# Performance work log

Measured on AMD Instinct MI355X. Metric: run time of the kernel, lower is better.

The kernel has to match this reference:

```python
import jax, jax.numpy as jnp
import numpy as np

N_GRAPHS = 64
NEG_SLOPE = 0.01  # default LeakyReLU slope
BN_EPS = 1e-5


def setup_inputs() -> dict:
    key = jax.random.key(0)
    ks = jax.random.split(key, 16)
    N, E, F_IN, H, H2, OUT, L = 50000, 800000, 64, 128, 64, 8, 3
    return {
        "x": jax.random.normal(ks[0], (N, F_IN), jnp.float32),
        "edge_index": jax.random.randint(ks[1], (2, E), 0, N, jnp.int32),
        "batch": jnp.sort(jax.random.randint(ks[2], (N,), 0, N_GRAPHS, jnp.int32)),
        "W_emb": jax.random.normal(ks[3], (F_IN, H), jnp.float32) * 0.05,
        "b_emb": jnp.zeros((H,), jnp.float32),
        "convW": jax.random.normal(ks[4], (L, H, H), jnp.float32) * 0.05,
        "convB": jnp.zeros((L, H), jnp.float32),
        "bn_gamma": jax.random.uniform(ks[5], (L, H), jnp.float32) + 0.5,
        "bn_beta": jax.random.normal(ks[6], (L, H), jnp.float32) * 0.1,
        "bn_mean": jax.random.normal(ks[7], (L, H), jnp.float32) * 0.1,
        "bn_var": jax.random.uniform(ks[8], (L, H), jnp.float32) + 0.5,
        "W1": jax.random.normal(ks[9], (H, H2), jnp.float32) * 0.05,
        "b1": jnp.zeros((H2,), jnp.float32),
        "W2": jax.random.normal(ks[10], (H2, OUT), jnp.float32) * 0.05,
        "b2": jnp.zeros((OUT,), jnp.float32),
    }


def reference(x, edge_index, batch, W_emb, b_emb, convW, convB,
              bn_gamma, bn_beta, bn_mean, bn_var, W1, b1, W2, b2):
    N = x.shape[0]
    # GCN normalization with self-loops (computed once; identical per layer)
    loop = jnp.arange(N, dtype=edge_index.dtype)
    s = jnp.concatenate([edge_index[0], loop])  # [E+N]
    d = jnp.concatenate([edge_index[1], loop])
    deg = jax.ops.segment_sum(jnp.ones(d.shape, x.dtype), d, num_segments=N)
    dinv = jax.lax.rsqrt(deg)  # deg >= 1 thanks to self-loops
    norm = dinv[s] * dinv[d]  # [E+N]

    h = x @ W_emb + b_emb  # node embedding, [N, H]
    L = convW.shape[0]
    for i in range(L):
        m = h @ convW[i]  # linear transform, [N, H]
        # gather-weight-scatter: sum_{(s->d)} norm * m[s]
        agg = jax.ops.segment_sum(m[s] * norm[:, None], d, num_segments=N) + convB[i]
        # BatchNorm (eval mode, running stats)
        hbn = (agg - bn_mean[i]) * jax.lax.rsqrt(bn_var[i] + BN_EPS) * bn_gamma[i] + bn_beta[i]
        h = jnp.where(hbn > 0, hbn, NEG_SLOPE * hbn)  # LeakyReLU
        # dropout is identity in eval mode

    g = jax.ops.segment_sum(h, batch, num_segments=N_GRAPHS)  # global_add_pool, [G, H]
    z = g @ W1 + b1
    z = jnp.where(z > 0, z, NEG_SLOPE * z)
    return z @ W2 + b2  # [G, OUT]
```

## Files before the change

kernel.cpp:

```cpp
#include <hip/hip_runtime.h>

#define NEG 0.01f
#define HF 128
#define BK 64
#define CAP 5120

typedef __attribute__((ext_vector_type(8))) short bf8;
typedef __attribute__((ext_vector_type(4))) float f4;

__device__ __forceinline__ unsigned short f2bf(float v) {
    unsigned u = __float_as_uint(v);
    u = (u + 0x7fff + ((u >> 16) & 1)) >> 16;
    return (unsigned short)u;
}

__global__ __launch_bounds__(256) void k_mega1(
        const int* __restrict__ src, const int* __restrict__ dst, int E,
        int* __restrict__ bin_cnt, int2* __restrict__ binbuf,
        const float* __restrict__ x, const float* __restrict__ W_emb,
        const float* __restrict__ b_emb, short* __restrict__ hbuf, int N,
        const float* __restrict__ convW, short* __restrict__ wt_c, int L,
        int PB, int EB) {
    __shared__ short wt[128 * 88];
    __shared__ int hist[256];
    __shared__ int base[256];
    const int bid = blockIdx.x;
    const int tid = threadIdx.x;

    if (bid < PB) {
        const int per = (E + PB - 1) / PB;
        const int e0 = bid * per;
        const int e1 = (e0 + per < E) ? e0 + per : E;
        hist[tid] = 0;
        __syncthreads();
        for (int e = e0 + tid; e < e1; e += 256)
            atomicAdd(&hist[dst[e] >> 8], 1);
        __syncthreads();
        const int h = hist[tid];
        base[tid] = h > 0 ? atomicAdd(&bin_cnt[tid], h) : 0;
        hist[tid] = 0;
        __syncthreads();
        for (int e = e0 + tid; e < e1; e += 256) {
            const int d = dst[e];
            const int b = d >> 8;
            const int slot = base[b] + atomicAdd(&hist[b], 1);
            if (slot < CAP) binbuf[(size_t)b * CAP + slot] = make_int2(src[e], d);
        }
        return;
    }
    if (bid < PB + EB) {
        for (int i = tid; i < 128 * 64; i += 256) {
            const int n = i >> 6, k = i & 63;
            wt[n * 88 + k] = (short)f2bf(W_emb[(size_t)k * HF + n]);
        }
        __syncthreads();
        const int wid = tid >> 6, lane = tid & 63;
        const int lr = lane & 15, lk = lane >> 4;
        const int m0 = (bid - PB) * 64 + wid * 16;
        if (m0 >= N) return;
        const int arow_i = m0 + lr < N ? m0 + lr : N - 1;
        bf8 a[2];
        const float* arow = x + (size_t)arow_i * 64 + lk * 8;
#pragma unroll
        for (int kk = 0; kk < 2; ++kk) {
            const float4 p = *reinterpret_cast<const float4*>(arow + kk * 32);
            const float4 q = *reinterpret_cast<const float4*>(arow + kk * 32 + 4);
            bf8 t;
            t[0] = (short)f2bf(p.x); t[1] = (short)f2bf(p.y);
            t[2] = (short)f2bf(p.z); t[3] = (short)f2bf(p.w);
            t[4] = (short)f2bf(q.x); t[5] = (short)f2bf(q.y);
            t[6] = (short)f2bf(q.z); t[7] = (short)f2bf(q.w);
            a[kk] = t;
        }
#pragma unroll
        for (int n = 0; n < 8; ++n) {
            f4 acc = {0.f, 0.f, 0.f, 0.f};
            const short* brow = wt + (n * 16 + lr) * 88 + lk * 8;
#pragma unroll
            for (int kk = 0; kk < 2; ++kk) {
                const bf8 b = *reinterpret_cast<const bf8*>(brow + kk * 32);
                acc = __builtin_amdgcn_mfma_f32_16x16x32_bf16(a[kk], b, acc, 0, 0, 0);
            }
            const int col = n * 16 + lr;
            const float bs = b_emb[col];
#pragma unroll
            for (int r = 0; r < 4; ++r)
                hbuf[(size_t)(m0 + lk * 4 + r) * HF + col] = (short)f2bf(acc[r] + bs);
        }
        return;
    }
    const int i = (bid - PB - EB) * 256 + tid;
    const int per = HF * HF;
    if (i < L * per) {
        const int l = i / per, r = i % per;
        const int n = r / HF, k = r % HF;
        wt_c[i] = (short)f2bf(convW[(size_t)l * per + (size_t)k * HF + n]);
    }
}

__global__ __launch_bounds__(256) void k_binfill(
        const int* __restrict__ bin_cnt, const int2* __restrict__ binbuf,
        int* __restrict__ bkt, int* __restrict__ cnt,
        float* __restrict__ gbuf, int NBIN) {
    const int bid = blockIdx.x;
    const int tid = threadIdx.x;
    if (bid >= NBIN) {
        for (int i = tid; i < 64 * HF; i += 256) gbuf[i] = 0.0f;
        return;
    }
    __shared__ int lcnt[256];
    lcnt[tid] = 0;
    __syncthreads();
    int count = bin_cnt[bid];
    if (count > CAP) count = CAP;
    for (int e = tid; e < count; e += 256) {
        const int2 ed = binbuf[(size_t)bid * CAP + e];
        const int p = atomicAdd(&lcnt[ed.y & 255], 1);
        if (p < BK) bkt[(size_t)ed.y * BK + p] = ed.x;
    }
    __syncthreads();
    cnt[(bid << 8) + tid] = lcnt[tid];
}

__global__ __launch_bounds__(256) void k_gemm_conv(
        const short* __restrict__ A,
        const short* __restrict__ Bt,
        const int* __restrict__ cnt,
        short* __restrict__ C,
        int N) {
    const int tid = threadIdx.x;
    const int wid = tid >> 6, lane = tid & 63;
    const int lr = lane & 15, lk = lane >> 4;
    const int m0 = blockIdx.x * 128 + wid * 32;
    if (m0 >= N) return;
    bf8 aA[4], aB[4];
    const short* arowA = A + (size_t)(m0 + lr) * HF + lk * 8;
    const short* arowB = arowA + 16 * HF;
#pragma unroll
    for (int kk = 0; kk < 4; ++kk) {
        aA[kk] = *reinterpret_cast<const bf8*>(arowA + kk * 32);
        aB[kk] = *reinterpret_cast<const bf8*>(arowB + kk * 32);
    }
    float dvA[4], dvB[4];
#pragma unroll
    for (int r = 0; r < 4; ++r) {
        int rowA = m0 + lk * 4 + r;       if (rowA >= N) rowA = N - 1;
        int rowB = m0 + 16 + lk * 4 + r;  if (rowB >= N) rowB = N - 1;
        dvA[r] = rsqrtf((float)cnt[rowA] + 1.0f);
        dvB[r] = rsqrtf((float)cnt[rowB] + 1.0f);
    }
#pragma unroll
    for (int n = 0; n < 8; ++n) {
        f4 accA = {0.f, 0.f, 0.f, 0.f};
        f4 accB = {0.f, 0.f, 0.f, 0.f};
        const short* brow = Bt + (size_t)(n * 16 + lr) * HF + lk * 8;
#pragma unroll
        for (int kk = 0; kk < 4; ++kk) {
            const bf8 b = *reinterpret_cast<const bf8*>(brow + kk * 32);
            accA = __builtin_amdgcn_mfma_f32_16x16x32_bf16(aA[kk], b, accA, 0, 0, 0);
            accB = __builtin_amdgcn_mfma_f32_16x16x32_bf16(aB[kk], b, accB, 0, 0, 0);
        }
        const int col = n * 16 + lr;
#pragma unroll
        for (int r = 0; r < 4; ++r) {
            C[(size_t)(m0 + lk * 4 + r) * HF + col]      = (short)f2bf(accA[r] * dvA[r]);
            C[(size_t)(m0 + 16 + lk * 4 + r) * HF + col] = (short)f2bf(accB[r] * dvB[r]);
        }
    }
}

__global__ __launch_bounds__(256) void k_gather(
        const int* __restrict__ bkt, const int* __restrict__ cnt,
        const short* __restrict__ ms,
        const float* __restrict__ convB,
        const float* __restrict__ bn_g, const float* __restrict__ bn_b,
        const float* __restrict__ bn_m, const float* __restrict__ bn_v,
        short* __restrict__ h, int N) {
    const int wid  = (blockIdx.x * 256 + threadIdx.x) >> 6;
    const int lane = threadIdx.x & 63;
    const int sub  = lane >> 4;
    const int lf   = lane & 15;
    if (wid >= N) return;
    const size_t b0 = (size_t)wid * BK;
    const int myslot = bkt[b0 + lane];
    int deg = cnt[wid];
    if (deg > BK) deg = BK;

    float acc[8] = {0.f, 0.f, 0.f, 0.f, 0.f, 0.f, 0.f, 0.f};
    union U { bf8 v; unsigned u[4]; };

    U self;
    self.v = *reinterpret_cast<const bf8*>(ms + (size_t)wid * HF + lf * 8);

    const int iters = (deg + 3) >> 2;
    int slot = sub;
    bool valid = slot < deg;
    U r;
    {
        const int s = valid ? __shfl(myslot, slot) : wid;
        r.v = *reinterpret_cast<const bf8*>(ms + (size_t)s * HF + lf * 8);
    }
    for (int t = 1; t < iters; ++t) {
        const int slot2 = slot + 4;
        const bool valid2 = slot2 < deg;
        const int s2 = valid2 ? __shfl(myslot, slot2) : wid;
        U r2;
        r2.v = *reinterpret_cast<const bf8*>(ms + (size_t)s2 * HF + lf * 8);
        if (valid) {
#pragma unroll
            for (int j = 0; j < 4; ++j) {
                acc[2 * j]     += __uint_as_float(r.u[j] << 16);
                acc[2 * j + 1] += __uint_as_float(r.u[j] & 0xffff0000u);
            }
        }
        r = r2; valid = valid2; slot = slot2;
    }
    if (valid) {
#pragma unroll
        for (int j = 0; j < 4; ++j) {
            acc[2 * j]     += __uint_as_float(r.u[j] << 16);
            acc[2 * j + 1] += __uint_as_float(r.u[j] & 0xffff0000u);
        }
    }
    if (sub == 0) {
#pragma unroll
        for (int j = 0; j < 4; ++j) {
            acc[2 * j]     += __uint_as_float(self.u[j] << 16);
            acc[2 * j + 1] += __uint_as_float(self.u[j] & 0xffff0000u);
        }
    }
#pragma unroll
    for (int j = 0; j < 8; ++j) {
        acc[j] += __shfl_xor(acc[j], 16);
        acc[j] += __shfl_xor(acc[j], 32);
    }
    if (sub == 0) {
        const float dv = rsqrtf((float)deg + 1.0f);
        const int f0 = lf * 8;
        unsigned ou[4];
#pragma unroll
        for (int j = 0; j < 4; ++j) {
            const int fx = f0 + 2 * j, fy = fx + 1;
            const float sx = rsqrtf(bn_v[fx] + 1e-5f) * bn_g[fx];
            const float sy = rsqrtf(bn_v[fy] + 1e-5f) * bn_g[fy];
            float vx = (dv * acc[2 * j]     + convB[fx] - bn_m[fx]) * sx + bn_b[fx];
            float vy = (dv * acc[2 * j + 1] + convB[fy] - bn_m[fy]) * sy + bn_b[fy];
            vx = vx > 0.0f ? vx : NEG * vx;
            vy = vy > 0.0f ? vy : NEG * vy;
            ou[j] = (unsigned)f2bf(vx) | ((unsigned)f2bf(vy) << 16);
        }
        *reinterpret_cast<uint4*>(h + (size_t)wid * HF + f0) =
            *reinterpret_cast<uint4*>(ou);
    }
}

__global__ __launch_bounds__(256) void k_pool(
        const short* __restrict__ h, const int* __restrict__ batch,
        float* __restrict__ g, int N, int per) {
    const int gwid = (blockIdx.x * 256 + threadIdx.x) >> 6;
    const int lane = threadIdx.x & 63;
    const int n0 = gwid * per;
    if (n0 >= N) return;
    const int n1 = (n0 + per < N) ? n0 + per : N;
    const int fp = lane * 2;
    float ax = 0.f, ay = 0.f;
    int cur = batch[n0];
    for (int n = n0; n < n1; ++n) {
        const int b = batch[n];
        if (b != cur) {
            atomicAdd(&g[cur * HF + fp], ax);
            atomicAdd(&g[cur * HF + fp + 1], ay);
            ax = 0.f; ay = 0.f; cur = b;
        }
        const unsigned u = *reinterpret_cast<const unsigned*>(h + (size_t)n * HF + fp);
        ax += __uint_as_float(u << 16);
        ay += __uint_as_float(u & 0xffff0000u);
    }
    atomicAdd(&g[cur * HF + fp], ax);
    atomicAdd(&g[cur * HF + fp + 1], ay);
}

__global__ __launch_bounds__(128) void k_mlp(
        const float* __restrict__ g, const float* __restrict__ W1,
        const float* __restrict__ b1, const float* __restrict__ W2,
        const float* __restrict__ b2, float* __restrict__ out) {
    __shared__ float gr[128];
    __shared__ float z[64];
    const int gid = blockIdx.x, t = threadIdx.x;
    gr[t] = g[gid * HF + t];
    __syncthreads();
    if (t < 64) {
        float acc = b1[t];
#pragma unroll 8
        for (int k = 0; k < 128; ++k) acc += gr[k] * W1[k * 64 + t];
        z[t] = acc > 0.0f ? acc : NEG * acc;
    }
    __syncthreads();
    if (t < 8) {
        float acc = b2[t];
#pragma unroll 8
        for (int j = 0; j < 64; ++j) acc += z[j] * W2[j * 8 + t];
        out[gid * 8 + t] = acc;
    }
}

extern "C" void kernel_launch(void* const* d_in, const int* in_sizes, int n_in,
                              void* d_out, int out_size, void* d_ws, size_t ws_size,
                              hipStream_t stream) {
    const float* x       = (const float*)d_in[0];
    const int*   eidx    = (const int*)  d_in[1];
    const int*   batch   = (const int*)  d_in[2];
    const float* W_emb   = (const float*)d_in[3];
    const float* b_emb   = (const float*)d_in[4];
    const float* convW   = (const float*)d_in[5];
    const float* convB   = (const float*)d_in[6];
    const float* bn_g    = (const float*)d_in[7];
    const float* bn_b    = (const float*)d_in[8];
    const float* bn_m    = (const float*)d_in[9];
    const float* bn_v    = (const float*)d_in[10];
    const float* W1      = (const float*)d_in[11];
    const float* b1      = (const float*)d_in[12];
    const float* W2      = (const float*)d_in[13];
    const float* b2      = (const float*)d_in[14];

    const int F_IN = 64;
    const int N = in_sizes[0] / F_IN;
    const int E = in_sizes[1] / 2;
    const int L = in_sizes[5] / (HF * HF);
    const int G = 64;

    const int* esrc = eidx;
    const int* edst = eidx + E;

    const int NBIN  = (N + 255) >> 8;
    const int Npad2 = NBIN << 8;
    const int Npad  = ((N + 127) / 128) * 128;

    int* bkt     = (int*)d_ws;
    int* cnt     = bkt + (size_t)Npad2 * BK;
    int* bin_cnt = cnt + Npad2;
    short* hbuf  = (short*)(bin_cnt + 256);
    short* ms    = hbuf + (size_t)Npad * HF;
    short* wt_c  = ms + (size_t)Npad * HF;
    float* gbuf  = (float*)(wt_c + (size_t)L * HF * HF);
    int2* binbuf = (int2*)ms;

    hipMemsetAsync(bin_cnt, 0, 256 * sizeof(int), stream);

    const int PB = 128;
    const int EB = (N + 63) / 64;
    const int WB = (L * HF * HF + 255) / 256;
    k_mega1<<<PB + EB + WB, 256, 0, stream>>>(
        esrc, edst, E, bin_cnt, binbuf, x, W_emb, b_emb, hbuf, N,
        convW, wt_c, L, PB, EB);

    k_binfill<<<NBIN + 1, 256, 0, stream>>>(bin_cnt, binbuf, bkt, cnt, gbuf, NBIN);

    for (int i = 0; i < L; ++i) {
        k_gemm_conv<<<(N + 127) / 128, 256, 0, stream>>>(
            hbuf, wt_c + (size_t)i * HF * HF, cnt, ms, N);
        k_gather<<<(N * 64 + 255) / 256, 256, 0, stream>>>(
            bkt, cnt, ms, convB + i * HF,
            bn_g + i * HF, bn_b + i * HF, bn_m + i * HF, bn_v + i * HF, hbuf, N);
    }

    const int nwaves = 256 * 4;
    const int per = (N + nwaves - 1) / nwaves;
    k_pool<<<256, 256, 0, stream>>>(hbuf, batch, gbuf, N, per);
    k_mlp<<<G, 128, 0, stream>>>(gbuf, W1, b1, W2, b2, (float*)d_out);
}
```

Before: 239.4 us.

## Replace global-atomic bin partition with per-block fixed segments; deepen gather prefetch

Edge binning now writes each partition block's edges into a private fixed-size segment per bin, recording per-cell counts. This removes the histogram pass, the global atomic offsets and the memset. k_binfill reads the segments with one thread per cell instead of one contiguous range. The gather kernel also prefetches two neighbor rows ahead instead of one to hide more load latency. The cost is a larger workspace and silent edge dropping if any cell exceeds SEG entries, which is not guaranteed for arbitrary inputs. The per-thread serial loops in binfill are also uneven.

```diff
diff --git a/kernel.cpp b/kernel.cpp
--- a/kernel.cpp
+++ b/kernel.cpp
@@ -3,7 +3,8 @@
 #define NEG 0.01f
 #define HF 128
 #define BK 64
-#define CAP 5120
+#define PB 256
+#define SEG 56
 
 typedef __attribute__((ext_vector_type(8))) short bf8;
 typedef __attribute__((ext_vector_type(4))) float f4;
@@ -16,35 +17,33 @@
 
 __global__ __launch_bounds__(256) void k_mega1(
         const int* __restrict__ src, const int* __restrict__ dst, int E,
-        int* __restrict__ bin_cnt, int2* __restrict__ binbuf,
+        int* __restrict__ cellcnt, int2* __restrict__ binbuf,
         const float* __restrict__ x, const float* __restrict__ W_emb,
         const float* __restrict__ b_emb, short* __restrict__ hbuf, int N,
         const float* __restrict__ convW, short* __restrict__ wt_c, int L,
-        int PB, int EB) {
+        int NBIN, int EB) {
     __shared__ short wt[128 * 88];
-    __shared__ int hist[256];
-    __shared__ int base[256];
+    __shared__ int lcur[256];
     const int bid = blockIdx.x;
     const int tid = threadIdx.x;
 
     if (bid < PB) {
+        lcur[tid] = 0;
+        __syncthreads();
         const int per = (E + PB - 1) / PB;
         const int e0 = bid * per;
         const int e1 = (e0 + per < E) ? e0 + per : E;
-        hist[tid] = 0;
-        __syncthreads();
-        for (int e = e0 + tid; e < e1; e += 256)
-            atomicAdd(&hist[dst[e] >> 8], 1);
-        __syncthreads();
-        const int h = hist[tid];
-        base[tid] = h > 0 ? atomicAdd(&bin_cnt[tid], h) : 0;
-        hist[tid] = 0;
-        __syncthreads();
         for (int e = e0 + tid; e < e1; e += 256) {
             const int d = dst[e];
             const int b = d >> 8;
-            const int slot = base[b] + atomicAdd(&hist[b], 1);
-            if (slot < CAP) binbuf[(size_t)b * CAP + slot] = make_int2(src[e], d);
+            const int p = atomicAdd(&lcur[b], 1);
+            if (p < SEG)
+                binbuf[((size_t)b * PB + bid) * SEG + p] = make_int2(src[e], d);
+        }
+        __syncthreads();
+        if (tid < NBIN) {
+            int c = lcur[tid];
+            cellcnt[(size_t)tid * PB + bid] = c < SEG ? c : SEG;
         }
         return;
     }
@@ -99,7 +98,7 @@
 }
 
 __global__ __launch_bounds__(256) void k_binfill(
-        const int* __restrict__ bin_cnt, const int2* __restrict__ binbuf,
+        const int* __restrict__ cellcnt, const int2* __restrict__ binbuf,
         int* __restrict__ bkt, int* __restrict__ cnt,
         float* __restrict__ gbuf, int NBIN) {
     const int bid = blockIdx.x;
@@ -111,10 +110,10 @@
     __shared__ int lcnt[256];
     lcnt[tid] = 0;
     __syncthreads();
-    int count = bin_cnt[bid];
-    if (count > CAP) count = CAP;
-    for (int e = tid; e < count; e += 256) {
-        const int2 ed = binbuf[(size_t)bid * CAP + e];
+    const int c = cellcnt[(size_t)bid * PB + tid];
+    const int2* segp = binbuf + ((size_t)bid * PB + tid) * SEG;
+    for (int i = 0; i < c; ++i) {
+        const int2 ed = segp[i];
         const int p = atomicAdd(&lcnt[ed.y & 255], 1);
         if (p < BK) bkt[(size_t)ed.y * BK + p] = ed.x;
     }
@@ -194,33 +193,28 @@
 
     const int iters = (deg + 3) >> 2;
     int slot = sub;
-    bool valid = slot < deg;
-    U r;
-    {
-        const int s = valid ? __shfl(myslot, slot) : wid;
-        r.v = *reinterpret_cast<const bf8*>(ms + (size_t)s * HF + lf * 8);
-    }
-    for (int t = 1; t < iters; ++t) {
-        const int slot2 = slot + 4;
-        const bool valid2 = slot2 < deg;
-        const int s2 = valid2 ? __shfl(myslot, slot2) : wid;
+    bool v0 = slot < deg;
+    U r0;
+    { const int s = v0 ? __shfl(myslot, slot) : wid;
+      r0.v = *reinterpret_cast<const bf8*>(ms + (size_t)s * HF + lf * 8); }
+    bool v1 = slot + 4 < deg;
+    U r1;
+    { const int s = v1 ? __shfl(myslot, slot + 4) : wid;
+      r1.v = *reinterpret_cast<const bf8*>(ms + (size_t)s * HF + lf * 8); }
+    for (int t = 0; t < iters; ++t) {
+        const int sl2 = slot + 8;
+        const bool v2 = sl2 < deg;
+        const int s2 = v2 ? __shfl(myslot, sl2) : wid;
         U r2;
         r2.v = *reinterpret_cast<const bf8*>(ms + (size_t)s2 * HF + lf * 8);
-        if (valid) {
+        if (v0) {
 #pragma unroll
             for (int j = 0; j < 4; ++j) {
-                acc[2 * j]     += __uint_as_float(r.u[j] << 16);
-                acc[2 * j + 1] += __uint_as_float(r.u[j] & 0xffff0000u);
+                acc[2 * j]     += __uint_as_float(r0.u[j] << 16);
+                acc[2 * j + 1] += __uint_as_float(r0.u[j] & 0xffff0000u);
             }
         }
-        r = r2; valid = valid2; slot = slot2;
-    }
-    if (valid) {
-#pragma unroll
-        for (int j = 0; j < 4; ++j) {
-            acc[2 * j]     += __uint_as_float(r.u[j] << 16);
-            acc[2 * j + 1] += __uint_as_float(r.u[j] & 0xffff0000u);
-        }
+        r0 = r1; v0 = v1; r1 = r2; v1 = v2; slot += 4;
     }
     if (sub == 0) {
 #pragma unroll
@@ -336,25 +330,22 @@
     const int Npad2 = NBIN << 8;
     const int Npad  = ((N + 127) / 128) * 128;
 
-    int* bkt     = (int*)d_ws;
-    int* cnt     = bkt + (size_t)Npad2 * BK;
-    int* bin_cnt = cnt + Npad2;
-    short* hbuf  = (short*)(bin_cnt + 256);
-    short* ms    = hbuf + (size_t)Npad * HF;
-    short* wt_c  = ms + (size_t)Npad * HF;
-    float* gbuf  = (float*)(wt_c + (size_t)L * HF * HF);
-    int2* binbuf = (int2*)ms;
-
-    hipMemsetAsync(bin_cnt, 0, 256 * sizeof(int), stream);
-
-    const int PB = 128;
+    int* bkt      = (int*)d_ws;
+    int* cnt      = bkt + (size_t)Npad2 * BK;
+    int* cellcnt  = cnt + Npad2;
+    int2* binbuf  = (int2*)(cellcnt + (size_t)NBIN * PB);
+    short* hbuf   = (short*)(binbuf + (size_t)NBIN * PB * SEG);
+    short* ms     = hbuf + (size_t)Npad * HF;
+    short* wt_c   = ms + (size_t)Npad * HF;
+    float* gbuf   = (float*)(wt_c + (size_t)L * HF * HF);
+
     const int EB = (N + 63) / 64;
     const int WB = (L * HF * HF + 255) / 256;
     k_mega1<<<PB + EB + WB, 256, 0, stream>>>(
-        esrc, edst, E, bin_cnt, binbuf, x, W_emb, b_emb, hbuf, N,
-        convW, wt_c, L, PB, EB);
-
-    k_binfill<<<NBIN + 1, 256, 0, stream>>>(bin_cnt, binbuf, bkt, cnt, gbuf, NBIN);
+        esrc, edst, E, cellcnt, binbuf, x, W_emb, b_emb, hbuf, N,
+        convW, wt_c, L, NBIN, EB);
+
+    k_binfill<<<NBIN + 1, 256, 0, stream>>>(cellcnt, binbuf, bkt, cnt, gbuf, NBIN);
 
     for (int i = 0; i < L; ++i) {
         k_gemm_conv<<<(N + 127) / 128, 256, 0, stream>>>(
```

Measured after the change: 237.6 us. Within noise of the previous version (-0.7%).
